# Kernel optimization log

Hardware: AMD Instinct MI355X
Metric: run time of the kernel (lower is better)

Reference implementation:

```python
import jax, jax.numpy as jnp
import numpy as np

NB = 64        # number of chains = batch.max()+1 (static for reshape)
NPER = 131072  # points per chain
NTYPES = 16
NITER = 10
ACC = 1e-9


def setup_inputs() -> dict:
    key = jax.random.key(0)
    k1, k2, k3 = jax.random.split(key, 3)
    x = jax.random.normal(k1, (NB * NPER, 3), dtype=jnp.float32)
    d0 = jax.random.uniform(k2, (NTYPES, NTYPES), dtype=jnp.float32, minval=0.5, maxval=1.5)
    z = jax.random.randint(k3, (NB * NPER,), 0, NTYPES)
    batch = jnp.repeat(jnp.arange(NB), NPER)  # contiguous chain ids
    return {"x": x, "d0": d0, "batch": batch, "z": z}


def _diffT(C):
    # adjoint of the forward difference stencil: [nb, n-1, 3] -> [nb, n, 3]
    mid = C[:, :-1] - C[:, 1:]
    return jnp.concatenate([-C[:, :1], mid, C[:, -1:]], axis=1)


def _constraint(r, d):
    # r: [nb, n, 3], d: [nb, n-1, 1]; c_i = |r_{i+1}-r_i|^2 - d_i^2
    dx = r[:, 1:] - r[:, :-1]
    c = jnp.sum(dx * dx, axis=-1, keepdims=True) - d * d
    return c, dx


def _line_search(x_sg, lam_sg, d_sg, alpha0, cnorm):
    # emulates the torch.no_grad() backtracking line search
    def eval_ctry(a):
        rt = (x_sg - a * lam_sg).reshape(NB, NPER, 3)
        ct, _ = _constraint(rt, d_sg)
        return jnp.sum(ct * ct)

    def cond(s):
        return ~s[3]

    def body(s):
        alpha, lsiter, _, _ = s
        ctry = eval_ctry(alpha)
        ok = ctry < cnorm
        new_alpha = jnp.where(ok, alpha, alpha * 0.5)
        new_lsiter = jnp.where(ok, lsiter, lsiter + 1)
        done = ok | (new_lsiter > 10)
        return (new_alpha, new_lsiter, ctry, done)

    init = (alpha0, jnp.int32(0), jnp.float32(jnp.inf), jnp.bool_(False))
    alpha, lsiter, ctry, _ = jax.lax.while_loop(cond, body, init)
    # if no backtracking happened and not converged, grow the step
    alpha = jnp.where((lsiter == 0) & (ctry > ACC), alpha * 1.5, alpha)
    return alpha, ctry


def _forward(x, d0, z):
    z2 = z.reshape(NB, NPER)
    # gather-based distance lookup for consecutive pairs: [NB, NPER-1, 1]
    d = d0[z2[:, :-1], z2[:, 1:]].astype(x.dtype)[..., None]
    d_sg = jax.lax.stop_gradient(d)
    x_cur = x
    alpha = jnp.float32(0.0)
    done = jnp.bool_(False)
    for j in range(NITER):
        r = x_cur.reshape(NB, NPER, 3)
        c, dx = _constraint(r, d)               # [NB, NPER-1, 1], [NB, NPER-1, 3]
        lam = 2.0 * _diffT(c * dx)              # dConstraintT2: [NB, NPER, 3]
        lam_x = lam.reshape(-1, 3)
        cnorm = jnp.sum(c * c)
        x_sg = jax.lax.stop_gradient(x_cur)
        lam_sg = jax.lax.stop_gradient(lam_x)
        cnorm_sg = jax.lax.stop_gradient(cnorm)
        alpha0 = (1.0 / jnp.linalg.norm(lam_sg)) if j == 0 else alpha
        alpha_j, ctry = _line_search(x_sg, lam_sg, d_sg, alpha0, cnorm_sg)
        x_new = x_cur - alpha_j * lam_x
        # freeze updates after convergence (emulates the torch early break)
        x_cur = jnp.where(done, x_cur, x_new)
        alpha = jnp.where(done, alpha, alpha_j)
        done = done | (ctry < ACC)
    return x_cur


def reference(x, d0, batch, z):
    # batch only encodes nb = batch.max()+1; layout is contiguous chains (static NB)
    return _forward(x, d0, z)
```

## Files before the change

kernel.cpp:

```cpp
#include <hip/hip_runtime.h>

#define NB 64
#define NPER 131072
#define NTYPES 16
#define ACCV 1e-9

#define TB 256
#define TILE_PTS 1024
#define TILES_PER_CHAIN (NPER / TILE_PTS)
#define TILES_TOTAL (NB * TILES_PER_CHAIN)
#define FBLOCKS 2048
#define TPB (TILES_TOTAL / FBLOCKS)
#define NTOT (NB * NPER)
#define FX_MAX (NTOT * 3 / 4)
#define ZX_MAX (NTOT / 4)
#define XS_F4 774
#define ZS_I4 258

struct PCState {
  double alpha;
  double alpha_step;
  int done;
  int do_update;
  unsigned ticket;
};

__device__ inline double wave_sum64(double v) {
  #pragma unroll
  for (int o = 32; o > 0; o >>= 1) v += __shfl_down(v, o, 64);
  return v;
}

__global__ void pc_init(PCState* st) {
  st->alpha = 0.0;
  st->alpha_step = 0.0;
  st->done = 0;
  st->do_update = 1;
  st->ticket = 0u;
}

template <int MODE>
__global__ __launch_bounds__(TB, 4) void pc_fused(
    const float* __restrict__ xin, float* __restrict__ xout,
    const int* __restrict__ zin, const float* __restrict__ d0,
    PCState* st, double* __restrict__ part, int iter) {
  __shared__ float4 xs4[XS_F4];
  __shared__ int4 zs4[ZS_I4];
  __shared__ float xn[(TILE_PTS + 3) * 3];
  __shared__ float ds2[TILE_PTS + 4];
  __shared__ float d0s[NTYPES * NTYPES];
  __shared__ double redl[5][TB / 64];
  __shared__ int islast;
  const float* xs = (const float*)xs4;
  const int* zs = (const int*)zs4;

  const int tid = threadIdx.x;
  d0s[tid] = d0[tid];
  const float alpha = (MODE == 0 || !st->do_update) ? 0.f : (float)st->alpha_step;
  const float4* x4 = (const float4*)xin;
  const int4* z4 = (const int4*)zin;

  double s0 = 0, s1 = 0, s2 = 0, s3 = 0, s4 = 0;
  float4 pf0, pf1, pf2, pf3 = make_float4(0.f, 0.f, 0.f, 0.f);
  int4 pz0, pz1 = make_int4(0, 0, 0, 0);

  auto pf_issue = [&](int tile) {
    const int b_ = tile / TILES_PER_CHAIN;
    const int p0_ = b_ * NPER + (tile % TILES_PER_CHAIN) * TILE_PTS - 4;
    const int fx0 = (p0_ * 3) >> 2;
    const int zx0 = p0_ >> 2;
    pf0 = x4[min(max(fx0 + tid, 0), FX_MAX - 1)];
    pf1 = x4[min(max(fx0 + 256 + tid, 0), FX_MAX - 1)];
    pf2 = x4[min(max(fx0 + 512 + tid, 0), FX_MAX - 1)];
    if (tid < XS_F4 - 768) pf3 = x4[min(max(fx0 + 768 + tid, 0), FX_MAX - 1)];
    pz0 = z4[min(max(zx0 + tid, 0), ZX_MAX - 1)];
    if (tid < ZS_I4 - 256) pz1 = z4[min(max(zx0 + 256 + tid, 0), ZX_MAX - 1)];
  };

  pf_issue(blockIdx.x * TPB);
  for (int tt = 0; tt < TPB; ++tt) {
    const int tile = blockIdx.x * TPB + tt;
    const int P0 = (tile % TILES_PER_CHAIN) * TILE_PTS;
    const int base = (tile / TILES_PER_CHAIN) * NPER;

    xs4[tid] = pf0; xs4[tid + 256] = pf1; xs4[tid + 512] = pf2;
    if (tid < XS_F4 - 768) xs4[tid + 768] = pf3;
    zs4[tid] = pz0;
    if (tid < ZS_I4 - 256) zs4[tid + 256] = pz1;
    __syncthreads();

    if (tt + 1 < TPB) pf_issue(tile + 1);
    for (int q = tid; q < TILE_PTS + 3; q += TB) {
      const int p = P0 - 1 + q;
      float Ca[2][3]; float dd2v[2];
      #pragma unroll
      for (int k = 0; k < 2; ++k) {
        const int j = p - 1 + k;
        const int xi = (q + 2 + k) * 3;
        if (j >= 0 && j <= NPER - 2) {
          const float ax = xs[xi + 3] - xs[xi + 0];
          const float ay = xs[xi + 4] - xs[xi + 1];
          const float az = xs[xi + 5] - xs[xi + 2];
          const float dd = d0s[zs[q + 2 + k] * NTYPES + zs[q + 3 + k]];
          dd2v[k] = dd * dd;
          const float c = ax * ax + ay * ay + az * az - dd2v[k];
          Ca[k][0] = c * ax; Ca[k][1] = c * ay; Ca[k][2] = c * az;
        } else {
          dd2v[k] = 0.f; Ca[k][0] = 0.f; Ca[k][1] = 0.f; Ca[k][2] = 0.f;
        }
      }
      if (MODE != 2) { ds2[q] = dd2v[0]; ds2[q + 1] = dd2v[1]; }
      const int xi = (q + 3) * 3;
      const float nx = xs[xi + 0] - alpha * 2.f * (Ca[0][0] - Ca[1][0]);
      const float ny = xs[xi + 1] - alpha * 2.f * (Ca[0][1] - Ca[1][1]);
      const float nz = xs[xi + 2] - alpha * 2.f * (Ca[0][2] - Ca[1][2]);
      if (MODE != 2) {
        const bool pv = (p >= 0) && (p < NPER);
        const int o = q * 3;
        xn[o + 0] = pv ? nx : 0.f;
        xn[o + 1] = pv ? ny : 0.f;
        xn[o + 2] = pv ? nz : 0.f;
      }
      if (MODE != 0 && p >= P0 && p < P0 + TILE_PTS) {
        const int g = (base + p) * 3;
        xout[g + 0] = nx; xout[g + 1] = ny; xout[g + 2] = nz;
      }
    }
    __syncthreads();

    if (MODE != 2) {
      float q0 = 0, q1 = 0, q2 = 0, q3 = 0, q4 = 0;
      for (int qq = tid; qq < TILE_PTS; qq += TB) {
        const int i = P0 + qq;
        if (i <= NPER - 2) {
          float CN[3][3]; float cI = 0.f, dxv[3] = {0.f, 0.f, 0.f};
          #pragma unroll
          for (int k = 0; k < 3; ++k) {
            const int j = i - 1 + k;
            if (j >= 0 && j <= NPER - 2) {
              const int o = (qq + k) * 3;
              const float ax = xn[o + 3] - xn[o + 0];
              const float ay = xn[o + 4] - xn[o + 1];
              const float az = xn[o + 5] - xn[o + 2];
              const float c = ax * ax + ay * ay + az * az - ds2[qq + k + 1];
              CN[k][0] = c * ax; CN[k][1] = c * ay; CN[k][2] = c * az;
              if (k == 1) { cI = c; dxv[0] = ax; dxv[1] = ay; dxv[2] = az; }
            } else {
              CN[k][0] = 0.f; CN[k][1] = 0.f; CN[k][2] = 0.f;
            }
          }
          const float gx = 2.f * (2.f * CN[1][0] - CN[0][0] - CN[2][0]);
          const float gy = 2.f * (2.f * CN[1][1] - CN[0][1] - CN[2][1]);
          const float gz = 2.f * (2.f * CN[1][2] - CN[0][2] - CN[2][2]);
          const float A = gx * gx + gy * gy + gz * gz;
          const float Bv = -2.f * (dxv[0] * gx + dxv[1] * gy + dxv[2] * gz);
          q0 += cI * cI;
          q1 += 2.f * cI * Bv;
          q2 += Bv * Bv + 2.f * cI * A;
          q3 += 2.f * A * Bv;
          q4 += A * A;
        }
      }
      s0 += (double)q0; s1 += (double)q1; s2 += (double)q2;
      s3 += (double)q3; s4 += (double)q4;
    }
  }

  if (MODE == 2) return;

  {
    double v[5] = {s0, s1, s2, s3, s4};
    const int wave = tid >> 6, lane = tid & 63;
    #pragma unroll
    for (int k = 0; k < 5; ++k) {
      const double w = wave_sum64(v[k]);
      if (lane == 0) redl[k][wave] = w;
    }
    __syncthreads();
    if (tid == 0) {
      #pragma unroll
      for (int k = 0; k < 5; ++k)
        part[k * FBLOCKS + blockIdx.x] =
            redl[k][0] + redl[k][1] + redl[k][2] + redl[k][3];
      __threadfence();
      const unsigned tk = atomicAdd(&st->ticket, 1u);
      islast = (tk == FBLOCKS - 1) ? 1 : 0;
    }
    __syncthreads();
    if (!islast) return;
  }

  __threadfence();
  {
    double v[5] = {0, 0, 0, 0, 0};
    for (int i = tid; i < FBLOCKS; i += TB) {
      #pragma unroll
      for (int k = 0; k < 5; ++k) v[k] += part[k * FBLOCKS + i];
    }
    const int wave = tid >> 6, lane = tid & 63;
    #pragma unroll
    for (int k = 0; k < 5; ++k) {
      const double w = wave_sum64(v[k]);
      if (lane == 0) redl[k][wave] = w;
    }
    __syncthreads();
    if (tid == 0) {
      double S[5];
      #pragma unroll
      for (int k = 0; k < 5; ++k)
        S[k] = redl[k][0] + redl[k][1] + redl[k][2] + redl[k][3];
      const double cnorm = S[0];
      double alpha2 = (iter == 0) ? 1.0 / sqrt(-0.5 * S[1]) : st->alpha;
      int lsiter = 0;
      double ctry;
      for (;;) {
        ctry = S[0] + alpha2 * (S[1] + alpha2 * (S[2] + alpha2 * (S[3] + alpha2 * S[4])));
        if (ctry < cnorm) break;
        alpha2 *= 0.5;
        if (++lsiter > 10) break;
      }
      if (lsiter == 0 && ctry > ACCV) alpha2 *= 1.5;
      const int done_prev = st->done;
      st->alpha_step = alpha2;
      st->do_update = done_prev ? 0 : 1;
      if (!done_prev) st->alpha = alpha2;
      st->done = done_prev | ((ctry < ACCV) ? 1 : 0);
      st->ticket = 0u;
    }
  }
}

extern "C" void kernel_launch(void* const* d_in, const int* in_sizes, int n_in,
                              void* d_out, int out_size, void* d_ws, size_t ws_size,
                              hipStream_t stream) {
  const float* d0 = (const float*)d_in[1];
  const int* z = (const int*)d_in[3];
  float* ping = (float*)d_in[0];
  float* dout = (float*)d_out;
  PCState* st = (PCState*)d_ws;
  double* part = (double*)((char*)d_ws + 256);
  const size_t xbytes = (size_t)NB * NPER * 3 * sizeof(float);

  hipMemcpyAsync(dout, ping, xbytes, hipMemcpyDeviceToDevice, stream);
  pc_init<<<1, 1, 0, stream>>>(st);
  pc_fused<0><<<FBLOCKS, TB, 0, stream>>>(dout, dout, z, d0, st, part, 0);
  float* a = dout;
  float* bufb = ping;
  for (int j = 1; j <= 9; ++j) {
    pc_fused<1><<<FBLOCKS, TB, 0, stream>>>(a, bufb, z, d0, st, part, j);
    float* tmp = a; a = bufb; bufb = tmp;
  }
  pc_fused<2><<<FBLOCKS, TB, 0, stream>>>(a, bufb, z, d0, st, part, 10);
}
```

Measured before the change: 1.329 ms.

## Replace LDS tiling with register-resident per-thread groups and wavefront shuffles

Each thread now owns four consecutive points, loaded as three float4 vectors. Neighbour points come from lane shuffles, with scalar global loads only at wavefront edges. This replaces the shared-memory tile staging and its per-tile barriers. Squared rest lengths are precomputed once into a scratch buffer, so the d0 gather is no longer repeated every iteration. The initial device-to-device copy is dropped because iteration 0 writes the output directly. In exchange, the batch input buffer is reused as scratch and each thread needs more registers.

```diff
diff --git a/kernel.cpp b/kernel.cpp
--- a/kernel.cpp
+++ b/kernel.cpp
@@ -6,16 +6,12 @@
 #define ACCV 1e-9
 
 #define TB 256
-#define TILE_PTS 1024
-#define TILES_PER_CHAIN (NPER / TILE_PTS)
-#define TILES_TOTAL (NB * TILES_PER_CHAIN)
-#define FBLOCKS 2048
-#define TPB (TILES_TOTAL / FBLOCKS)
+#define GPC (NPER / 4)
+#define NGROUP (NB * GPC)
 #define NTOT (NB * NPER)
-#define FX_MAX (NTOT * 3 / 4)
-#define ZX_MAX (NTOT / 4)
-#define XS_F4 774
-#define ZS_I4 258
+#define FB 2048
+#define TPB (NGROUP / (FB * TB))
+#define DSQB (NGROUP / TB)
 
 struct PCState {
   double alpha;
@@ -39,138 +35,150 @@
   st->ticket = 0u;
 }
 
+__global__ __launch_bounds__(TB) void pc_dsq(const int* __restrict__ z,
+    const float* __restrict__ d0, float* __restrict__ dsq) {
+  const int T = blockIdx.x * TB + threadIdx.x;
+  const int gi = T & (GPC - 1);
+  const int4 zo = ((const int4*)z)[T];
+  int z4n = __shfl_down(zo.x, 1, 64);
+  if ((threadIdx.x & 63) == 63) z4n = z[min(4 * T + 4, NTOT - 1)];
+  float4 r;
+  float dd;
+  dd = d0[zo.x * NTYPES + zo.y]; r.x = dd * dd;
+  dd = d0[zo.y * NTYPES + zo.z]; r.y = dd * dd;
+  dd = d0[zo.z * NTYPES + zo.w]; r.z = dd * dd;
+  if (gi != GPC - 1) { dd = d0[zo.w * NTYPES + z4n]; r.w = dd * dd; }
+  else r.w = 0.f;
+  ((float4*)dsq)[T] = r;
+}
+
 template <int MODE>
-__global__ __launch_bounds__(TB, 4) void pc_fused(
+__global__ __launch_bounds__(TB) void pc_fused(
     const float* __restrict__ xin, float* __restrict__ xout,
-    const int* __restrict__ zin, const float* __restrict__ d0,
-    PCState* st, double* __restrict__ part, int iter) {
-  __shared__ float4 xs4[XS_F4];
-  __shared__ int4 zs4[ZS_I4];
-  __shared__ float xn[(TILE_PTS + 3) * 3];
-  __shared__ float ds2[TILE_PTS + 4];
-  __shared__ float d0s[NTYPES * NTYPES];
+    const float* __restrict__ dsq, PCState* st,
+    double* __restrict__ part, int iter) {
   __shared__ double redl[5][TB / 64];
   __shared__ int islast;
-  const float* xs = (const float*)xs4;
-  const int* zs = (const int*)zs4;
-
   const int tid = threadIdx.x;
-  d0s[tid] = d0[tid];
-  const float alpha = (MODE == 0 || !st->do_update) ? 0.f : (float)st->alpha_step;
+  const int lane = tid & 63;
+  const float alpha = (iter == 0 || !st->do_update) ? 0.f : (float)st->alpha_step;
   const float4* x4 = (const float4*)xin;
-  const int4* z4 = (const int4*)zin;
+  float4* o4 = (float4*)xout;
+  const float4* q4 = (const float4*)dsq;
 
   double s0 = 0, s1 = 0, s2 = 0, s3 = 0, s4 = 0;
-  float4 pf0, pf1, pf2, pf3 = make_float4(0.f, 0.f, 0.f, 0.f);
-  int4 pz0, pz1 = make_int4(0, 0, 0, 0);
-
-  auto pf_issue = [&](int tile) {
-    const int b_ = tile / TILES_PER_CHAIN;
-    const int p0_ = b_ * NPER + (tile % TILES_PER_CHAIN) * TILE_PTS - 4;
-    const int fx0 = (p0_ * 3) >> 2;
-    const int zx0 = p0_ >> 2;
-    pf0 = x4[min(max(fx0 + tid, 0), FX_MAX - 1)];
-    pf1 = x4[min(max(fx0 + 256 + tid, 0), FX_MAX - 1)];
-    pf2 = x4[min(max(fx0 + 512 + tid, 0), FX_MAX - 1)];
-    if (tid < XS_F4 - 768) pf3 = x4[min(max(fx0 + 768 + tid, 0), FX_MAX - 1)];
-    pz0 = z4[min(max(zx0 + tid, 0), ZX_MAX - 1)];
-    if (tid < ZS_I4 - 256) pz1 = z4[min(max(zx0 + 256 + tid, 0), ZX_MAX - 1)];
-  };
-
-  pf_issue(blockIdx.x * TPB);
+
+  int T = blockIdx.x * TPB * TB + tid;
+  float4 c0 = x4[3 * T], c1 = x4[3 * T + 1], c2 = x4[3 * T + 2];
+  float4 cq = q4[T];
+
   for (int tt = 0; tt < TPB; ++tt) {
-    const int tile = blockIdx.x * TPB + tt;
-    const int P0 = (tile % TILES_PER_CHAIN) * TILE_PTS;
-    const int base = (tile / TILES_PER_CHAIN) * NPER;
-
-    xs4[tid] = pf0; xs4[tid + 256] = pf1; xs4[tid + 512] = pf2;
-    if (tid < XS_F4 - 768) xs4[tid + 768] = pf3;
-    zs4[tid] = pz0;
-    if (tid < ZS_I4 - 256) zs4[tid + 256] = pz1;
-    __syncthreads();
-
-    if (tt + 1 < TPB) pf_issue(tile + 1);
-    for (int q = tid; q < TILE_PTS + 3; q += TB) {
-      const int p = P0 - 1 + q;
-      float Ca[2][3]; float dd2v[2];
-      #pragma unroll
-      for (int k = 0; k < 2; ++k) {
-        const int j = p - 1 + k;
-        const int xi = (q + 2 + k) * 3;
-        if (j >= 0 && j <= NPER - 2) {
-          const float ax = xs[xi + 3] - xs[xi + 0];
-          const float ay = xs[xi + 4] - xs[xi + 1];
-          const float az = xs[xi + 5] - xs[xi + 2];
-          const float dd = d0s[zs[q + 2 + k] * NTYPES + zs[q + 3 + k]];
-          dd2v[k] = dd * dd;
-          const float c = ax * ax + ay * ay + az * az - dd2v[k];
-          Ca[k][0] = c * ax; Ca[k][1] = c * ay; Ca[k][2] = c * az;
-        } else {
-          dd2v[k] = 0.f; Ca[k][0] = 0.f; Ca[k][1] = 0.f; Ca[k][2] = 0.f;
-        }
+    float4 n0 = c0, n1 = c1, n2 = c2, nq = cq;
+    if (tt + 1 < TPB) {
+      const int Tn = T + TB;
+      n0 = x4[3 * Tn]; n1 = x4[3 * Tn + 1]; n2 = x4[3 * Tn + 2];
+      nq = q4[Tn];
+    }
+    const int gi = T & (GPC - 1);
+    const int P0 = gi * 4;
+
+    float X[9][3];
+    X[2][0] = c0.x; X[2][1] = c0.y; X[2][2] = c0.z;
+    X[3][0] = c0.w; X[3][1] = c1.x; X[3][2] = c1.y;
+    X[4][0] = c1.z; X[4][1] = c1.w; X[4][2] = c2.x;
+    X[5][0] = c2.y; X[5][1] = c2.z; X[5][2] = c2.w;
+    X[0][0] = __shfl_up(c1.z, 1, 64); X[0][1] = __shfl_up(c1.w, 1, 64); X[0][2] = __shfl_up(c2.x, 1, 64);
+    X[1][0] = __shfl_up(c2.y, 1, 64); X[1][1] = __shfl_up(c2.z, 1, 64); X[1][2] = __shfl_up(c2.w, 1, 64);
+    X[6][0] = __shfl_down(c0.x, 1, 64); X[6][1] = __shfl_down(c0.y, 1, 64); X[6][2] = __shfl_down(c0.z, 1, 64);
+    X[7][0] = __shfl_down(c0.w, 1, 64); X[7][1] = __shfl_down(c1.x, 1, 64); X[7][2] = __shfl_down(c1.y, 1, 64);
+    X[8][0] = __shfl_down(c1.z, 1, 64); X[8][1] = __shfl_down(c1.w, 1, 64); X[8][2] = __shfl_down(c2.x, 1, 64);
+    float D[8];
+    D[2] = cq.x; D[3] = cq.y; D[4] = cq.z; D[5] = cq.w;
+    D[0] = __shfl_up(cq.z, 1, 64);  D[1] = __shfl_up(cq.w, 1, 64);
+    D[6] = __shfl_down(cq.x, 1, 64); D[7] = __shfl_down(cq.y, 1, 64);
+    if (lane == 0) {
+      const int fb = 12 * T;
+      #pragma unroll
+      for (int k = 0; k < 6; ++k)
+        X[k / 3][k % 3] = xin[max(fb - 6 + k, 0)];
+      D[0] = dsq[max(4 * T - 2, 0)];
+      D[1] = dsq[max(4 * T - 1, 0)];
+    }
+    if (lane == 63) {
+      const int fb = 12 * T + 12;
+      #pragma unroll
+      for (int k = 0; k < 9; ++k)
+        X[6 + k / 3][k % 3] = xin[min(fb + k, NTOT * 3 - 1)];
+      D[6] = dsq[min(4 * T + 4, NTOT - 1)];
+      D[7] = dsq[min(4 * T + 5, NTOT - 1)];
+    }
+
+    float Cold[8][3];
+    #pragma unroll
+    for (int m = 0; m < 8; ++m) {
+      const int j = P0 - 2 + m;
+      const float ax = X[m + 1][0] - X[m][0];
+      const float ay = X[m + 1][1] - X[m][1];
+      const float az = X[m + 1][2] - X[m][2];
+      const float cc = ax * ax + ay * ay + az * az - D[m];
+      const float cv = (j >= 0 && j <= NPER - 2) ? cc : 0.f;
+      Cold[m][0] = cv * ax; Cold[m][1] = cv * ay; Cold[m][2] = cv * az;
+    }
+    float XN[7][3];
+    #pragma unroll
+    for (int m = 0; m < 7; ++m) {
+      #pragma unroll
+      for (int e = 0; e < 3; ++e)
+        XN[m][e] = X[m + 1][e] - alpha * 2.f * (Cold[m][e] - Cold[m + 1][e]);
+    }
+    o4[3 * T + 0] = make_float4(XN[1][0], XN[1][1], XN[1][2], XN[2][0]);
+    o4[3 * T + 1] = make_float4(XN[2][1], XN[2][2], XN[3][0], XN[3][1]);
+    o4[3 * T + 2] = make_float4(XN[3][2], XN[4][0], XN[4][1], XN[4][2]);
+
+    if (MODE != 2) {
+      float CN[6][3], cnv[6], dXN[6][3];
+      #pragma unroll
+      for (int m = 0; m < 6; ++m) {
+        const int j = P0 - 1 + m;
+        const float ax = XN[m + 1][0] - XN[m][0];
+        const float ay = XN[m + 1][1] - XN[m][1];
+        const float az = XN[m + 1][2] - XN[m][2];
+        const float cc = ax * ax + ay * ay + az * az - D[m + 1];
+        const float cv = (j >= 0 && j <= NPER - 2) ? cc : 0.f;
+        cnv[m] = cv;
+        dXN[m][0] = ax; dXN[m][1] = ay; dXN[m][2] = az;
+        CN[m][0] = cv * ax; CN[m][1] = cv * ay; CN[m][2] = cv * az;
       }
-      if (MODE != 2) { ds2[q] = dd2v[0]; ds2[q + 1] = dd2v[1]; }
-      const int xi = (q + 3) * 3;
-      const float nx = xs[xi + 0] - alpha * 2.f * (Ca[0][0] - Ca[1][0]);
-      const float ny = xs[xi + 1] - alpha * 2.f * (Ca[0][1] - Ca[1][1]);
-      const float nz = xs[xi + 2] - alpha * 2.f * (Ca[0][2] - Ca[1][2]);
-      if (MODE != 2) {
-        const bool pv = (p >= 0) && (p < NPER);
-        const int o = q * 3;
-        xn[o + 0] = pv ? nx : 0.f;
-        xn[o + 1] = pv ? ny : 0.f;
-        xn[o + 2] = pv ? nz : 0.f;
-      }
-      if (MODE != 0 && p >= P0 && p < P0 + TILE_PTS) {
-        const int g = (base + p) * 3;
-        xout[g + 0] = nx; xout[g + 1] = ny; xout[g + 2] = nz;
-      }
-    }
-    __syncthreads();
-
-    if (MODE != 2) {
-      float q0 = 0, q1 = 0, q2 = 0, q3 = 0, q4 = 0;
-      for (int qq = tid; qq < TILE_PTS; qq += TB) {
-        const int i = P0 + qq;
-        if (i <= NPER - 2) {
-          float CN[3][3]; float cI = 0.f, dxv[3] = {0.f, 0.f, 0.f};
-          #pragma unroll
-          for (int k = 0; k < 3; ++k) {
-            const int j = i - 1 + k;
-            if (j >= 0 && j <= NPER - 2) {
-              const int o = (qq + k) * 3;
-              const float ax = xn[o + 3] - xn[o + 0];
-              const float ay = xn[o + 4] - xn[o + 1];
-              const float az = xn[o + 5] - xn[o + 2];
-              const float c = ax * ax + ay * ay + az * az - ds2[qq + k + 1];
-              CN[k][0] = c * ax; CN[k][1] = c * ay; CN[k][2] = c * az;
-              if (k == 1) { cI = c; dxv[0] = ax; dxv[1] = ay; dxv[2] = az; }
-            } else {
-              CN[k][0] = 0.f; CN[k][1] = 0.f; CN[k][2] = 0.f;
-            }
-          }
-          const float gx = 2.f * (2.f * CN[1][0] - CN[0][0] - CN[2][0]);
-          const float gy = 2.f * (2.f * CN[1][1] - CN[0][1] - CN[2][1]);
-          const float gz = 2.f * (2.f * CN[1][2] - CN[0][2] - CN[2][2]);
+      float q0 = 0, q1 = 0, q2 = 0, q3 = 0, q4v = 0;
+      #pragma unroll
+      for (int d = 0; d < 4; ++d) {
+        if (P0 + d <= NPER - 2) {
+          const int m = d + 1;
+          const float gx = 2.f * (2.f * CN[m][0] - CN[m - 1][0] - CN[m + 1][0]);
+          const float gy = 2.f * (2.f * CN[m][1] - CN[m - 1][1] - CN[m + 1][1]);
+          const float gz = 2.f * (2.f * CN[m][2] - CN[m - 1][2] - CN[m + 1][2]);
           const float A = gx * gx + gy * gy + gz * gz;
-          const float Bv = -2.f * (dxv[0] * gx + dxv[1] * gy + dxv[2] * gz);
+          const float Bv = -2.f * (dXN[m][0] * gx + dXN[m][1] * gy + dXN[m][2] * gz);
+          const float cI = cnv[m];
           q0 += cI * cI;
           q1 += 2.f * cI * Bv;
           q2 += Bv * Bv + 2.f * cI * A;
           q3 += 2.f * A * Bv;
-          q4 += A * A;
+          q4v += A * A;
         }
       }
       s0 += (double)q0; s1 += (double)q1; s2 += (double)q2;
-      s3 += (double)q3; s4 += (double)q4;
-    }
+      s3 += (double)q3; s4 += (double)q4v;
+    }
+
+    T += TB; c0 = n0; c1 = n1; c2 = n2; cq = nq;
   }
 
   if (MODE == 2) return;
 
   {
     double v[5] = {s0, s1, s2, s3, s4};
-    const int wave = tid >> 6, lane = tid & 63;
+    const int wave = tid >> 6;
     #pragma unroll
     for (int k = 0; k < 5; ++k) {
       const double w = wave_sum64(v[k]);
@@ -180,11 +188,11 @@
     if (tid == 0) {
       #pragma unroll
       for (int k = 0; k < 5; ++k)
-        part[k * FBLOCKS + blockIdx.x] =
+        part[k * FB + blockIdx.x] =
             redl[k][0] + redl[k][1] + redl[k][2] + redl[k][3];
       __threadfence();
       const unsigned tk = atomicAdd(&st->ticket, 1u);
-      islast = (tk == FBLOCKS - 1) ? 1 : 0;
+      islast = (tk == FB - 1) ? 1 : 0;
     }
     __syncthreads();
     if (!islast) return;
@@ -193,11 +201,11 @@
   __threadfence();
   {
     double v[5] = {0, 0, 0, 0, 0};
-    for (int i = tid; i < FBLOCKS; i += TB) {
-      #pragma unroll
-      for (int k = 0; k < 5; ++k) v[k] += part[k * FBLOCKS + i];
-    }
-    const int wave = tid >> 6, lane = tid & 63;
+    for (int i = tid; i < FB; i += TB) {
+      #pragma unroll
+      for (int k = 0; k < 5; ++k) v[k] += part[k * FB + i];
+    }
+    const int wave = tid >> 6;
     #pragma unroll
     for (int k = 0; k < 5; ++k) {
       const double w = wave_sum64(v[k]);
@@ -235,20 +243,19 @@
                               hipStream_t stream) {
   const float* d0 = (const float*)d_in[1];
   const int* z = (const int*)d_in[3];
-  float* ping = (float*)d_in[0];
-  float* dout = (float*)d_out;
+  float* IN = (float*)d_in[0];
+  float* dsq = (float*)d_in[2];
+  float* OUT = (float*)d_out;
   PCState* st = (PCState*)d_ws;
   double* part = (double*)((char*)d_ws + 256);
-  const size_t xbytes = (size_t)NB * NPER * 3 * sizeof(float);
-
-  hipMemcpyAsync(dout, ping, xbytes, hipMemcpyDeviceToDevice, stream);
+
   pc_init<<<1, 1, 0, stream>>>(st);
-  pc_fused<0><<<FBLOCKS, TB, 0, stream>>>(dout, dout, z, d0, st, part, 0);
-  float* a = dout;
-  float* bufb = ping;
-  for (int j = 1; j <= 9; ++j) {
-    pc_fused<1><<<FBLOCKS, TB, 0, stream>>>(a, bufb, z, d0, st, part, j);
-    float* tmp = a; a = bufb; bufb = tmp;
-  }
-  pc_fused<2><<<FBLOCKS, TB, 0, stream>>>(a, bufb, z, d0, st, part, 10);
-}
+  pc_dsq<<<DSQB, TB, 0, stream>>>(z, d0, dsq);
+  float* a = IN;
+  float* b = OUT;
+  for (int j = 0; j <= 9; ++j) {
+    pc_fused<1><<<FB, TB, 0, stream>>>(a, b, dsq, st, part, j);
+    float* t = a; a = b; b = t;
+  }
+  pc_fused<2><<<FB, TB, 0, stream>>>(a, b, dsq, st, part, 10);
+}
```

After: 1.690 ms. +27.2%, slower.

## Precompute squared bond lengths once and fold the initial copy into iteration zero

Applied to the files above, without the earlier changes.

A new pre-pass kernel gathers d0 for each consecutive pair into a float buffer of squared distances, stored in the otherwise unused batch input buffer. The fused kernel then loads these values directly instead of loading z, doing the d0 table lookup and staging ds2 in LDS, which also lowers shared-memory use. The device-to-device memcpy is removed: the first iteration now runs the normal update path with alpha set to zero, so it copies x into the output as it goes. The grid is also doubled to 4096 blocks with fewer tiles per block. The trade-off is an extra small launch and writing into an input buffer as scratch.

```diff
diff --git a/kernel.cpp b/kernel.cpp
--- a/kernel.cpp
+++ b/kernel.cpp
@@ -9,13 +9,15 @@
 #define TILE_PTS 1024
 #define TILES_PER_CHAIN (NPER / TILE_PTS)
 #define TILES_TOTAL (NB * TILES_PER_CHAIN)
-#define FBLOCKS 2048
+#define FBLOCKS 4096
 #define TPB (TILES_TOTAL / FBLOCKS)
 #define NTOT (NB * NPER)
-#define FX_MAX (NTOT * 3 / 4)
-#define ZX_MAX (NTOT / 4)
+#define NX4 (NTOT * 3 / 4)
+#define NQ4 (NTOT / 4)
 #define XS_F4 774
-#define ZS_I4 258
+#define QS_F4 258
+#define GPC (NPER / 4)
+#define DSQB (NTOT / 4 / TB)
 
 struct PCState {
   double alpha;
@@ -39,42 +41,57 @@
   st->ticket = 0u;
 }
 
+__global__ __launch_bounds__(TB) void pc_dsq(const int* __restrict__ z,
+    const float* __restrict__ d0, float* __restrict__ dsq) {
+  const int T = blockIdx.x * TB + threadIdx.x;
+  const int gi = T & (GPC - 1);
+  const int4 zo = ((const int4*)z)[T];
+  int z4n = __shfl_down(zo.x, 1, 64);
+  if ((threadIdx.x & 63) == 63) z4n = z[min(4 * T + 4, NTOT - 1)];
+  float4 r;
+  float dd;
+  dd = d0[zo.x * NTYPES + zo.y]; r.x = dd * dd;
+  dd = d0[zo.y * NTYPES + zo.z]; r.y = dd * dd;
+  dd = d0[zo.z * NTYPES + zo.w]; r.z = dd * dd;
+  if (gi != GPC - 1) { dd = d0[zo.w * NTYPES + z4n]; r.w = dd * dd; }
+  else r.w = 0.f;
+  ((float4*)dsq)[T] = r;
+}
+
 template <int MODE>
 __global__ __launch_bounds__(TB, 4) void pc_fused(
     const float* __restrict__ xin, float* __restrict__ xout,
-    const int* __restrict__ zin, const float* __restrict__ d0,
-    PCState* st, double* __restrict__ part, int iter) {
+    const float* __restrict__ dsq, PCState* st,
+    double* __restrict__ part, int iter) {
   __shared__ float4 xs4[XS_F4];
-  __shared__ int4 zs4[ZS_I4];
+  __shared__ float4 qs4[QS_F4];
   __shared__ float xn[(TILE_PTS + 3) * 3];
-  __shared__ float ds2[TILE_PTS + 4];
-  __shared__ float d0s[NTYPES * NTYPES];
   __shared__ double redl[5][TB / 64];
   __shared__ int islast;
   const float* xs = (const float*)xs4;
-  const int* zs = (const int*)zs4;
+  const float* qf = (const float*)qs4;
 
   const int tid = threadIdx.x;
-  d0s[tid] = d0[tid];
-  const float alpha = (MODE == 0 || !st->do_update) ? 0.f : (float)st->alpha_step;
+  const int lane = tid & 63;
+  const float alpha = (iter == 0 || !st->do_update) ? 0.f : (float)st->alpha_step;
   const float4* x4 = (const float4*)xin;
-  const int4* z4 = (const int4*)zin;
+  const float4* q4 = (const float4*)dsq;
 
   double s0 = 0, s1 = 0, s2 = 0, s3 = 0, s4 = 0;
   float4 pf0, pf1, pf2, pf3 = make_float4(0.f, 0.f, 0.f, 0.f);
-  int4 pz0, pz1 = make_int4(0, 0, 0, 0);
+  float4 pq0, pq1 = make_float4(0.f, 0.f, 0.f, 0.f);
 
   auto pf_issue = [&](int tile) {
     const int b_ = tile / TILES_PER_CHAIN;
     const int p0_ = b_ * NPER + (tile % TILES_PER_CHAIN) * TILE_PTS - 4;
     const int fx0 = (p0_ * 3) >> 2;
-    const int zx0 = p0_ >> 2;
-    pf0 = x4[min(max(fx0 + tid, 0), FX_MAX - 1)];
-    pf1 = x4[min(max(fx0 + 256 + tid, 0), FX_MAX - 1)];
-    pf2 = x4[min(max(fx0 + 512 + tid, 0), FX_MAX - 1)];
-    if (tid < XS_F4 - 768) pf3 = x4[min(max(fx0 + 768 + tid, 0), FX_MAX - 1)];
-    pz0 = z4[min(max(zx0 + tid, 0), ZX_MAX - 1)];
-    if (tid < ZS_I4 - 256) pz1 = z4[min(max(zx0 + 256 + tid, 0), ZX_MAX - 1)];
+    const int qx0 = p0_ >> 2;
+    pf0 = x4[min(max(fx0 + tid, 0), NX4 - 1)];
+    pf1 = x4[min(max(fx0 + 256 + tid, 0), NX4 - 1)];
+    pf2 = x4[min(max(fx0 + 512 + tid, 0), NX4 - 1)];
+    if (tid < XS_F4 - 768) pf3 = x4[min(max(fx0 + 768 + tid, 0), NX4 - 1)];
+    pq0 = q4[min(max(qx0 + tid, 0), NQ4 - 1)];
+    if (tid < QS_F4 - 256) pq1 = q4[min(max(qx0 + 256 + tid, 0), NQ4 - 1)];
   };
 
   pf_issue(blockIdx.x * TPB);
@@ -85,14 +102,14 @@
 
     xs4[tid] = pf0; xs4[tid + 256] = pf1; xs4[tid + 512] = pf2;
     if (tid < XS_F4 - 768) xs4[tid + 768] = pf3;
-    zs4[tid] = pz0;
-    if (tid < ZS_I4 - 256) zs4[tid + 256] = pz1;
+    qs4[tid] = pq0;
+    if (tid < QS_F4 - 256) qs4[tid + 256] = pq1;
     __syncthreads();
 
     if (tt + 1 < TPB) pf_issue(tile + 1);
     for (int q = tid; q < TILE_PTS + 3; q += TB) {
       const int p = P0 - 1 + q;
-      float Ca[2][3]; float dd2v[2];
+      float Ca[2][3];
       #pragma unroll
       for (int k = 0; k < 2; ++k) {
         const int j = p - 1 + k;
@@ -101,15 +118,12 @@
           const float ax = xs[xi + 3] - xs[xi + 0];
           const float ay = xs[xi + 4] - xs[xi + 1];
           const float az = xs[xi + 5] - xs[xi + 2];
-          const float dd = d0s[zs[q + 2 + k] * NTYPES + zs[q + 3 + k]];
-          dd2v[k] = dd * dd;
-          const float c = ax * ax + ay * ay + az * az - dd2v[k];
+          const float c = ax * ax + ay * ay + az * az - qf[q + k + 2];
           Ca[k][0] = c * ax; Ca[k][1] = c * ay; Ca[k][2] = c * az;
         } else {
-          dd2v[k] = 0.f; Ca[k][0] = 0.f; Ca[k][1] = 0.f; Ca[k][2] = 0.f;
+          Ca[k][0] = 0.f; Ca[k][1] = 0.f; Ca[k][2] = 0.f;
         }
       }
-      if (MODE != 2) { ds2[q] = dd2v[0]; ds2[q + 1] = dd2v[1]; }
       const int xi = (q + 3) * 3;
       const float nx = xs[xi + 0] - alpha * 2.f * (Ca[0][0] - Ca[1][0]);
       const float ny = xs[xi + 1] - alpha * 2.f * (Ca[0][1] - Ca[1][1]);
@@ -129,7 +143,7 @@
     __syncthreads();
 
     if (MODE != 2) {
-      float q0 = 0, q1 = 0, q2 = 0, q3 = 0, q4 = 0;
+      float q0 = 0, q1 = 0, q2 = 0, q3 = 0, q4v = 0;
       for (int qq = tid; qq < TILE_PTS; qq += TB) {
         const int i = P0 + qq;
         if (i <= NPER - 2) {
@@ -142,7 +156,7 @@
               const float ax = xn[o + 3] - xn[o + 0];
               const float ay = xn[o + 4] - xn[o + 1];
               const float az = xn[o + 5] - xn[o + 2];
-              const float c = ax * ax + ay * ay + az * az - ds2[qq + k + 1];
+              const float c = ax * ax + ay * ay + az * az - qf[qq + k + 3];
               CN[k][0] = c * ax; CN[k][1] = c * ay; CN[k][2] = c * az;
               if (k == 1) { cI = c; dxv[0] = ax; dxv[1] = ay; dxv[2] = az; }
             } else {
@@ -158,11 +172,11 @@
           q1 += 2.f * cI * Bv;
           q2 += Bv * Bv + 2.f * cI * A;
           q3 += 2.f * A * Bv;
-          q4 += A * A;
+          q4v += A * A;
         }
       }
       s0 += (double)q0; s1 += (double)q1; s2 += (double)q2;
-      s3 += (double)q3; s4 += (double)q4;
+      s3 += (double)q3; s4 += (double)q4v;
     }
   }
 
@@ -170,7 +184,7 @@
 
   {
     double v[5] = {s0, s1, s2, s3, s4};
-    const int wave = tid >> 6, lane = tid & 63;
+    const int wave = tid >> 6;
     #pragma unroll
     for (int k = 0; k < 5; ++k) {
       const double w = wave_sum64(v[k]);
@@ -197,7 +211,7 @@
       #pragma unroll
       for (int k = 0; k < 5; ++k) v[k] += part[k * FBLOCKS + i];
     }
-    const int wave = tid >> 6, lane = tid & 63;
+    const int wave = tid >> 6;
     #pragma unroll
     for (int k = 0; k < 5; ++k) {
       const double w = wave_sum64(v[k]);
@@ -235,20 +249,19 @@
                               hipStream_t stream) {
   const float* d0 = (const float*)d_in[1];
   const int* z = (const int*)d_in[3];
-  float* ping = (float*)d_in[0];
-  float* dout = (float*)d_out;
+  float* IN = (float*)d_in[0];
+  float* dsq = (float*)d_in[2];
+  float* OUT = (float*)d_out;
   PCState* st = (PCState*)d_ws;
   double* part = (double*)((char*)d_ws + 256);
-  const size_t xbytes = (size_t)NB * NPER * 3 * sizeof(float);
-
-  hipMemcpyAsync(dout, ping, xbytes, hipMemcpyDeviceToDevice, stream);
+
   pc_init<<<1, 1, 0, stream>>>(st);
-  pc_fused<0><<<FBLOCKS, TB, 0, stream>>>(dout, dout, z, d0, st, part, 0);
-  float* a = dout;
-  float* bufb = ping;
-  for (int j = 1; j <= 9; ++j) {
-    pc_fused<1><<<FBLOCKS, TB, 0, stream>>>(a, bufb, z, d0, st, part, j);
-    float* tmp = a; a = bufb; bufb = tmp;
-  }
-  pc_fused<2><<<FBLOCKS, TB, 0, stream>>>(a, bufb, z, d0, st, part, 10);
-}
+  pc_dsq<<<DSQB, TB, 0, stream>>>(z, d0, dsq);
+  float* a = IN;
+  float* b = OUT;
+  for (int j = 0; j <= 9; ++j) {
+    pc_fused<1><<<FBLOCKS, TB, 0, stream>>>(a, b, dsq, st, part, j);
+    float* t = a; a = b; b = t;
+  }
+  pc_fused<2><<<FBLOCKS, TB, 0, stream>>>(a, b, dsq, st, part, 10);
+}
```

Measured after the change: 1.985 ms. 49.4% more time.
